# Kernel tuning notes

Hardware: AMD Instinct MI355X
Metric: run time of the kernel (lower is better)

The kernel has to match this reference:

```python
import jax, jax.numpy as jnp
import numpy as np

B, HIDDEN, NH, MAX_S = 8, 4096, 32, 4096
HD = HIDDEN // NH  # 128
POS = 2047  # current cache write position (tokens 0..POS-1 already cached)


def setup_inputs() -> dict:
    key = jax.random.key(0)
    ks = jax.random.split(key, 7)
    x = jax.random.normal(ks[0], (B, 1, HIDDEN), dtype=jnp.float32)
    cached_k = jax.random.normal(ks[1], (B, NH, MAX_S, HD), dtype=jnp.float32)
    cached_v = jax.random.normal(ks[2], (B, NH, MAX_S, HD), dtype=jnp.float32)
    scale = 0.02
    wq = jax.random.normal(ks[3], (HIDDEN, HIDDEN), dtype=jnp.float32) * scale
    wk = jax.random.normal(ks[4], (HIDDEN, HIDDEN), dtype=jnp.float32) * scale
    wv = jax.random.normal(ks[5], (HIDDEN, HIDDEN), dtype=jnp.float32) * scale
    wo = jax.random.normal(ks[6], (HIDDEN, HIDDEN), dtype=jnp.float32) * scale
    return {"x": x, "cached_k": cached_k, "cached_v": cached_v,
            "wq": wq, "wk": wk, "wv": wv, "wo": wo, "cached_pos": POS}


def reference(x, cached_k, cached_v, wq, wk, wv, wo, cached_pos):
    # Decode step: seq_len == 1 (is_training=False path of the torch module).
    b, s, hidden = x.shape  # s == 1
    # Projections (torch Linear: y = x @ W.T), reshape to [B, H, 1, D]
    q = (x @ wq.T).reshape(b, s, NH, HD).transpose(0, 2, 1, 3)
    k = (x @ wk.T).reshape(b, s, NH, HD).transpose(0, 2, 1, 3)
    v = (x @ wv.T).reshape(b, s, NH, HD).transpose(0, 2, 1, 3)
    # Append new token's K/V into the cache at cached_pos (static python int)
    ck = cached_k.at[:, :, cached_pos, :].set(k[:, :, 0, :])
    cv = cached_v.at[:, :, cached_pos, :].set(v[:, :, 0, :])
    # Attend over the valid prefix [0, cached_pos]
    kk = ck[:, :, :cached_pos + 1, :]  # [B, H, T, D]
    vv = cv[:, :, :cached_pos + 1, :]
    scores = jnp.einsum('bhqd,bhkd->bhqk', q, kk) / jnp.sqrt(jnp.float32(HD))
    att = jax.nn.softmax(scores, axis=-1)  # stable softmax == module's _softmax
    out = jnp.einsum('bhqk,bhkd->bhqd', att, vv)  # [B, H, 1, D]
    out = out.transpose(0, 2, 1, 3).reshape(b, s, hidden)
    return out @ wo.T
```

## Files before the change

### kernel.cpp

```cpp
#include <hip/hip_runtime.h>
#include <cmath>

#define B_     8
#define NH_    32
#define HD_    128
#define HID_   4096
#define MAXS_  4096
#define NPAIR_ (B_ * NH_)
#define NSPLIT_ 4
#define PSTR_  132
#define QS_    (3 * B_ * HID_)
#define NEG_BIG_ (-1e30f)

typedef float f4_ __attribute__((ext_vector_type(4)));

__device__ __forceinline__ f4_ ntload4(const float* p) {
  return __builtin_nontemporal_load((const f4_*)p);
}
__device__ __forceinline__ f4_ ld4(const float* p) {
  return *(const f4_*)p;
}
__device__ __forceinline__ float dot4(f4_ a, f4_ b) {
  f4_ m = a * b;
  return m.x + m.y + m.z + m.w;
}

template<int NSL>
__global__ __launch_bounds__(64) void gemv_ks(
    const float* __restrict__ W0, const float* __restrict__ W1,
    const float* __restrict__ W2, const float* __restrict__ x,
    float* __restrict__ out, int nb_per_mat, int n_inner, int part_stride)
{
  const int bid   = blockIdx.x;
  const int ks    = bid / n_inner;
  const int inner = bid % n_inner;
  const int m     = inner / nb_per_mat;
  const int r0    = (inner % nb_per_mat) * 8;
  const float* __restrict__ W = (m == 0) ? W0 : ((m == 1) ? W1 : W2);
  float* o = out + (size_t)ks * part_stride + m * (B_ * HID_);

  const int lane = threadIdx.x;
  const int kofs = ks * NSL * 256;

  float acc[8][8];
#pragma unroll
  for (int r = 0; r < 8; ++r)
#pragma unroll
    for (int b = 0; b < 8; ++b) acc[r][b] = 0.f;

  const float* Wp = W + (size_t)r0 * HID_ + kofs + lane * 4;
  const float* xp = x + kofs + lane * 4;

  f4_ wa[8], wb[8];
#pragma unroll
  for (int r = 0; r < 8; ++r) wa[r] = ld4(Wp + (size_t)r * HID_);

#pragma unroll 1
  for (int u = 0; u < NSL; u += 2) {
    {
      const int j = u * 256;
      f4_ xv[8];
#pragma unroll
      for (int b = 0; b < 8; ++b) xv[b] = ld4(xp + b * HID_ + j);
#pragma unroll
      for (int r = 0; r < 8; ++r)
        wb[r] = ld4(Wp + (size_t)r * HID_ + j + 256);
#pragma unroll
      for (int r = 0; r < 8; ++r)
#pragma unroll
        for (int b = 0; b < 8; ++b) acc[r][b] += dot4(wa[r], xv[b]);
    }
    {
      const int j = (u + 1) * 256;
      f4_ xv[8];
#pragma unroll
      for (int b = 0; b < 8; ++b) xv[b] = ld4(xp + b * HID_ + j);
      if (u + 2 < NSL) {
#pragma unroll
        for (int r = 0; r < 8; ++r)
          wa[r] = ld4(Wp + (size_t)r * HID_ + j + 256);
      }
#pragma unroll
      for (int r = 0; r < 8; ++r)
#pragma unroll
        for (int b = 0; b < 8; ++b) acc[r][b] += dot4(wb[r], xv[b]);
    }
  }

#pragma unroll
  for (int r = 0; r < 8; ++r)
#pragma unroll
    for (int b = 0; b < 8; ++b) {
      float v = acc[r][b];
#pragma unroll
      for (int off = 32; off; off >>= 1) v += __shfl_xor(v, off);
      acc[r][b] = v;
    }

  if (lane == 0) {
#pragma unroll
    for (int r = 0; r < 8; ++r)
#pragma unroll
      for (int b = 0; b < 8; ++b)
        o[(size_t)b * HID_ + r0 + r] = acc[r][b];
  }
}

__global__ __launch_bounds__(256) void sum4(
    const float* __restrict__ part, float* __restrict__ out)
{
  const int gid = blockIdx.x * 256 + threadIdx.x;
  const int i = gid * 4;
  f4_ v = ld4(part + i) + ld4(part + (B_ * HID_) + i)
        + ld4(part + 2 * (B_ * HID_) + i) + ld4(part + 3 * (B_ * HID_) + i);
  *(f4_*)(out + i) = v;
}

__global__ __launch_bounds__(256, 4) void attn_partial(
    const float* __restrict__ qkv, const float* __restrict__ ck,
    const float* __restrict__ cv, const int* __restrict__ ppos,
    float* __restrict__ part)
{
  __shared__ float sm[4], sl[4];
  __shared__ float sacc[4][HD_];

  const int pos  = *ppos;
  const int bid  = blockIdx.x;
  const int pair = bid >> 2;
  const int s    = bid & (NSPLIT_ - 1);
  const int b    = pair >> 5;
  const int h    = pair & (NH_ - 1);
  const int w    = threadIdx.x >> 6;
  const int lane = threadIdx.x & 63;
  const int half = lane >> 5, l32 = lane & 31;
  const int k0   = s * 512 + w * 128;

  float m = NEG_BIG_, l = 0.f;
  f4_ acc = (f4_)0.f;

  if (k0 <= pos) {
    const float scale = 0.08838834764831845f;
    const int hoff = b * HID_ + h * HD_ + l32 * 4;
    f4_ q4  = (ld4(qkv + hoff) + ld4(qkv + QS_ + hoff)) * scale;
    f4_ kf4 =  ld4(qkv + B_ * HID_ + hoff) + ld4(qkv + QS_ + B_ * HID_ + hoff);
    f4_ vf4 =  ld4(qkv + 2 * B_ * HID_ + hoff) + ld4(qkv + QS_ + 2 * B_ * HID_ + hoff);
    const float* ckh = ck + ((size_t)(b * NH_ + h)) * MAXS_ * HD_;
    const float* cvh = cv + ((size_t)(b * NH_ + h)) * MAXS_ * HD_;

    for (int c = 0; c < 8; ++c) {
      const int kbase = k0 + c * 16;
      f4_ k4[8], v4[8];
#pragma unroll
      for (int j = 0; j < 8; ++j) {
        const int ki = kbase + 2 * j + half;
        k4[j] = ntload4(ckh + (size_t)ki * HD_ + l32 * 4);
        v4[j] = ntload4(cvh + (size_t)ki * HD_ + l32 * 4);
      }
#pragma unroll
      for (int j = 0; j < 8; ++j) {
        const int ki = kbase + 2 * j + half;
        if (ki == pos) { k4[j] = kf4; v4[j] = vf4; }
      }

      float sc[8];
#pragma unroll
      for (int j = 0; j < 8; ++j) sc[j] = dot4(q4, k4[j]);

#pragma unroll
      for (int off = 16; off >= 1; off >>= 1)
#pragma unroll
        for (int j = 0; j < 8; ++j) sc[j] += __shfl_xor(sc[j], off);

#pragma unroll
      for (int j = 0; j < 8; ++j) {
        const int ki = kbase + 2 * j + half;
        if (ki > pos) sc[j] = -INFINITY;
      }

      const float cm = fmaxf(fmaxf(fmaxf(sc[0], sc[1]), fmaxf(sc[2], sc[3])),
                             fmaxf(fmaxf(sc[4], sc[5]), fmaxf(sc[6], sc[7])));
      const float mn   = fmaxf(m, cm);
      const float corr = __expf(m - mn);
      float p[8], ps = 0.f;
#pragma unroll
      for (int j = 0; j < 8; ++j) { p[j] = __expf(sc[j] - mn); ps += p[j]; }
      l = l * corr + ps;
      acc *= corr;
#pragma unroll
      for (int j = 0; j < 8; ++j) acc += p[j] * v4[j];
      m = mn;
    }
  }

  const float mo = __shfl_xor(m, 32);
  const float lo = __shfl_xor(l, 32);
  f4_ ao;
  ao.x = __shfl_xor(acc.x, 32); ao.y = __shfl_xor(acc.y, 32);
  ao.z = __shfl_xor(acc.z, 32); ao.w = __shfl_xor(acc.w, 32);
  const float mm = fmaxf(m, mo);
  const float w0 = __expf(m - mm), w1 = __expf(mo - mm);
  const float lm = l * w0 + lo * w1;
  f4_ am = acc * w0 + ao * w1;

  if (half == 0) {
    *(f4_*)&sacc[w][l32 * 4] = am;
    if (l32 == 0) { sm[w] = mm; sl[w] = lm; }
  }
  __syncthreads();

  if (threadIdx.x < 32) {
    const int t = threadIdx.x;
    float mg = NEG_BIG_;
#pragma unroll
    for (int u = 0; u < 4; ++u)
      if (sl[u] > 0.f) mg = fmaxf(mg, sm[u]);
    float ls = 0.f;
    f4_ o = (f4_)0.f;
#pragma unroll
    for (int u = 0; u < 4; ++u)
      if (sl[u] > 0.f) {
        const float wu = __expf(sm[u] - mg);
        ls += sl[u] * wu;
        o  += wu * ld4(&sacc[u][t * 4]);
      }
    float* pb = part + (size_t)bid * PSTR_;
    *(f4_*)(pb + 4 + t * 4) = o;
    if (t == 0) { pb[0] = (ls > 0.f) ? mg : NEG_BIG_; pb[1] = ls; }
  }
}

__global__ __launch_bounds__(128) void attn_combine(
    const float* __restrict__ part, float* __restrict__ attnout)
{
  const int pair = blockIdx.x;
  const int d    = threadIdx.x;
  const float* pb = part + (size_t)pair * NSPLIT_ * PSTR_;

  float mg = NEG_BIG_;
#pragma unroll
  for (int u = 0; u < NSPLIT_; ++u) {
    const float lu = pb[u * PSTR_ + 1];
    if (lu > 0.f) mg = fmaxf(mg, pb[u * PSTR_]);
  }
  float ls = 0.f, o = 0.f;
#pragma unroll
  for (int u = 0; u < NSPLIT_; ++u) {
    const float lu = pb[u * PSTR_ + 1];
    if (lu > 0.f) {
      const float wu = __expf(pb[u * PSTR_] - mg);
      ls += lu * wu;
      o  += wu * pb[u * PSTR_ + 4 + d];
    }
  }
  attnout[pair * HD_ + d] = o / ls;
}

extern "C" void kernel_launch(void* const* d_in, const int* in_sizes, int n_in,
                              void* d_out, int out_size, void* d_ws, size_t ws_size,
                              hipStream_t stream) {
  const float* x  = (const float*)d_in[0];
  const float* ck = (const float*)d_in[1];
  const float* cv = (const float*)d_in[2];
  const float* wq = (const float*)d_in[3];
  const float* wk = (const float*)d_in[4];
  const float* wv = (const float*)d_in[5];
  const float* wo = (const float*)d_in[6];
  const int* pos  = (const int*)d_in[7];
  float* out = (float*)d_out;
  float* ws  = (float*)d_ws;

  float* qkvp    = ws;
  float* part    = qkvp + 2 * QS_;
  float* attnout = part + NPAIR_ * NSPLIT_ * PSTR_;
  float* wopart  = attnout + B_ * HID_;

  gemv_ks<8><<<2 * 3 * 512, 64, 0, stream>>>(wq, wk, wv, x, qkvp,
                                             512, 3 * 512, QS_);
  attn_partial<<<NPAIR_ * NSPLIT_, 256, 0, stream>>>(qkvp, ck, cv, pos, part);
  attn_combine<<<NPAIR_, 128, 0, stream>>>(part, attnout);
  gemv_ks<4><<<4 * 512, 64, 0, stream>>>(wo, wo, wo, attnout, wopart,
                                         512, 512, B_ * HID_);
  sum4<<<(B_ * HID_) / (256 * 4), 256, 0, stream>>>(wopart, out);
}
```

Measured before the change: 182.4 us.

## Share staged activation tiles across four waves via LDS in GEMV kernels

The projection GEMV kernels now run four waves per block, each handling 8 output rows, so a block covers 32 rows. The activation slice for each k-step is loaded once per block into double-buffered shared memory with global_load_lds and then read by all four waves, where before every 64-thread block reloaded it from global memory. This cuts redundant x traffic. In exchange it adds two __syncthreads per step and 16KB of LDS per block, which may lower occupancy.

```diff
diff --git a/kernel.cpp b/kernel.cpp
--- a/kernel.cpp
+++ b/kernel.cpp
@@ -1,5 +1,6 @@
 #include <hip/hip_runtime.h>
 #include <cmath>
+#include <cstdint>
 
 #define B_     8
 #define NH_    32
@@ -25,22 +26,32 @@
   return m.x + m.y + m.z + m.w;
 }
 
+__device__ __forceinline__ void stage16(const float* gsrc, unsigned ldsoff) {
+  __builtin_amdgcn_global_load_lds(
+      (__attribute__((address_space(1))) void*)(uintptr_t)gsrc,
+      (__attribute__((address_space(3))) void*)ldsoff,
+      16, 0, 0);
+}
+
 template<int NSL>
-__global__ __launch_bounds__(64) void gemv_ks(
+__global__ __launch_bounds__(256) void gemv_shx(
     const float* __restrict__ W0, const float* __restrict__ W1,
     const float* __restrict__ W2, const float* __restrict__ x,
     float* __restrict__ out, int nb_per_mat, int n_inner, int part_stride)
 {
+  extern __shared__ float dyn[];
   const int bid   = blockIdx.x;
   const int ks    = bid / n_inner;
   const int inner = bid % n_inner;
   const int m     = inner / nb_per_mat;
-  const int r0    = (inner % nb_per_mat) * 8;
+  const int r0    = (inner % nb_per_mat) * 32;
   const float* __restrict__ W = (m == 0) ? W0 : ((m == 1) ? W1 : W2);
   float* o = out + (size_t)ks * part_stride + m * (B_ * HID_);
 
-  const int lane = threadIdx.x;
+  const int wib  = threadIdx.x >> 6;
+  const int lane = threadIdx.x & 63;
   const int kofs = ks * NSL * 256;
+  const int rw   = r0 + wib * 8;
 
   float acc[8][8];
 #pragma unroll
@@ -48,44 +59,59 @@
 #pragma unroll
     for (int b = 0; b < 8; ++b) acc[r][b] = 0.f;
 
-  const float* Wp = W + (size_t)r0 * HID_ + kofs + lane * 4;
+  const float* Wp = W + (size_t)rw * HID_ + kofs + lane * 4;
   const float* xp = x + kofs + lane * 4;
 
   f4_ wa[8], wb[8];
-#pragma unroll
-  for (int r = 0; r < 8; ++r) wa[r] = ld4(Wp + (size_t)r * HID_);
+
+#define XSTAGE_(buf, u)                                                       \
+  {                                                                           \
+    const int b0 = 2 * wib;                                                   \
+    stage16(xp + (size_t)b0 * HID_ + (u) * 256,                               \
+            (unsigned)((buf) * 8192 + b0 * 1024));                            \
+    stage16(xp + (size_t)(b0 + 1) * HID_ + (u) * 256,                         \
+            (unsigned)((buf) * 8192 + (b0 + 1) * 1024));                      \
+  }
+
+#define WPRE_(BUF, u)                                                         \
+  {                                                                           \
+    _Pragma("unroll")                                                         \
+    for (int r = 0; r < 8; ++r)                                               \
+      BUF[r] = ld4(Wp + (size_t)r * HID_ + (u) * 256);                        \
+  }
+
+#define COMP_(BUF, buf)                                                       \
+  {                                                                           \
+    f4_ xv[8];                                                                \
+    _Pragma("unroll")                                                         \
+    for (int b = 0; b < 8; ++b)                                               \
+      xv[b] = ld4(&dyn[(buf) * 2048 + b * 256 + lane * 4]);                   \
+    _Pragma("unroll")                                                         \
+    for (int r = 0; r < 8; ++r)                                               \
+      _Pragma("unroll")                                                       \
+      for (int b = 0; b < 8; ++b) acc[r][b] += dot4(BUF[r], xv[b]);           \
+  }
+
+  WPRE_(wa, 0);
+  XSTAGE_(0, 0);
+  __syncthreads();
 
 #pragma unroll 1
   for (int u = 0; u < NSL; u += 2) {
-    {
-      const int j = u * 256;
-      f4_ xv[8];
-#pragma unroll
-      for (int b = 0; b < 8; ++b) xv[b] = ld4(xp + b * HID_ + j);
-#pragma unroll
-      for (int r = 0; r < 8; ++r)
-        wb[r] = ld4(Wp + (size_t)r * HID_ + j + 256);
-#pragma unroll
-      for (int r = 0; r < 8; ++r)
-#pragma unroll
-        for (int b = 0; b < 8; ++b) acc[r][b] += dot4(wa[r], xv[b]);
+    WPRE_(wb, u + 1);
+    XSTAGE_(1, u + 1);
+    COMP_(wa, 0);
+    __syncthreads();
+    if (u + 2 < NSL) {
+      WPRE_(wa, u + 2);
+      XSTAGE_(0, u + 2);
     }
-    {
-      const int j = (u + 1) * 256;
-      f4_ xv[8];
-#pragma unroll
-      for (int b = 0; b < 8; ++b) xv[b] = ld4(xp + b * HID_ + j);
-      if (u + 2 < NSL) {
-#pragma unroll
-        for (int r = 0; r < 8; ++r)
-          wa[r] = ld4(Wp + (size_t)r * HID_ + j + 256);
-      }
-#pragma unroll
-      for (int r = 0; r < 8; ++r)
-#pragma unroll
-        for (int b = 0; b < 8; ++b) acc[r][b] += dot4(wb[r], xv[b]);
-    }
-  }
+    COMP_(wb, 1);
+    __syncthreads();
+  }
+#undef XSTAGE_
+#undef WPRE_
+#undef COMP_
 
 #pragma unroll
   for (int r = 0; r < 8; ++r)
@@ -102,7 +128,7 @@
     for (int r = 0; r < 8; ++r)
 #pragma unroll
       for (int b = 0; b < 8; ++b)
-        o[(size_t)b * HID_ + r0 + r] = acc[r][b];
+        o[(size_t)b * HID_ + rw + r] = acc[r][b];
   }
 }
 
@@ -274,11 +300,11 @@
   float* attnout = part + NPAIR_ * NSPLIT_ * PSTR_;
   float* wopart  = attnout + B_ * HID_;
 
-  gemv_ks<8><<<2 * 3 * 512, 64, 0, stream>>>(wq, wk, wv, x, qkvp,
-                                             512, 3 * 512, QS_);
+  gemv_shx<8><<<2 * 3 * 128, 256, 16384, stream>>>(wq, wk, wv, x, qkvp,
+                                                   128, 3 * 128, QS_);
   attn_partial<<<NPAIR_ * NSPLIT_, 256, 0, stream>>>(qkvp, ck, cv, pos, part);
   attn_combine<<<NPAIR_, 128, 0, stream>>>(part, attnout);
-  gemv_ks<4><<<4 * 512, 64, 0, stream>>>(wo, wo, wo, attnout, wopart,
-                                         512, 512, B_ * HID_);
+  gemv_shx<4><<<4 * 128, 256, 16384, stream>>>(wo, wo, wo, attnout, wopart,
+                                               128, 128, B_ * HID_);
   sum4<<<(B_ * HID_) / (256 * 4), 256, 0, stream>>>(wopart, out);
 }
```

After: 180.5 us. Within noise of the previous version (-1.0%).
